# Kernel tuning notes

Measured on AMD Instinct MI355X. Metric: run time of the kernel, lower is better.

The kernel has to match this reference:

```python
import jax, jax.numpy as jnp
import numpy as np

H = 256
I = 32
O = 10


def setup_inputs() -> dict:
    key = jax.random.key(0)
    ks = jax.random.split(key, 16)
    stdv = 1.0 / np.sqrt(H)
    u = lambda k, shape: jax.random.uniform(k, shape, jnp.float32, -stdv, stdv)
    x = jax.random.normal(ks[0], (256, 512, I), jnp.float32)
    return {
        "x": x,
        "Wgx": u(ks[1], (I, H)), "Wgh": u(ks[2], (H, H)), "bg": u(ks[3], (H,)),
        "Wix": u(ks[4], (I, H)), "Wih": u(ks[5], (H, H)), "bi": u(ks[6], (H,)),
        "Wfx": u(ks[7], (I, H)), "Wfh": u(ks[8], (H, H)), "bf": u(ks[9], (H,)),
        "Wox": u(ks[10], (I, H)), "Woh": u(ks[11], (H, H)), "bo": u(ks[12], (H,)),
        "Wph": u(ks[13], (H, O)), "bp": u(ks[14], (O,)),
    }


def _lstm_forward(x, Wgx, Wgh, bg, Wix, Wih, bi, Wfx, Wfh, bf, Wox, Woh, bo, Wph, bp):
    B, S, _ = x.shape
    # Precompute all input projections in one big GEMM: (B,S,I) @ (I,4H) -> (B,S,4H)
    Wx = jnp.concatenate([Wgx, Wix, Wfx, Wox], axis=1)      # (I, 4H)
    bx = jnp.concatenate([bg, bi, bf, bo], axis=0)          # (4H,)
    xproj = jnp.einsum("bsi,ik->bsk", x, Wx) + bx           # (B, S, 4H)
    Wh = jnp.concatenate([Wgh, Wih, Wfh, Woh], axis=1)      # (H, 4H)

    # Note: torch code skips the h@Wh term at t=0; with h0=c0=0 the math is identical.
    def step(carry, xp_t):
        h, c = carry
        z = xp_t + h @ Wh                                   # (B, 4H)
        g = jnp.tanh(z[:, 0 * H:1 * H])
        i = jax.nn.sigmoid(z[:, 1 * H:2 * H])
        f = jax.nn.sigmoid(z[:, 2 * H:3 * H])
        o = jax.nn.sigmoid(z[:, 3 * H:4 * H])
        c = g * i + c * f
        h = jnp.tanh(c) * o
        return (h, c), None

    h0 = jnp.zeros((B, H), x.dtype)
    c0 = jnp.zeros((B, H), x.dtype)
    (h, _), _ = jax.lax.scan(step, (h0, c0), jnp.swapaxes(xproj, 0, 1))
    out = h @ Wph + bp                                      # (B, O)
    return jax.nn.softmax(out, axis=1)


def reference(x, Wgx, Wgh, bg, Wix, Wih, bi, Wfx, Wfh, bf, Wox, Woh, bo, Wph, bp):
    return _lstm_forward(x, Wgx, Wgh, bg, Wix, Wih, bi, Wfx, Wfh, bf, Wox, Woh, bo, Wph, bp)
```

## Files before the change

kernel.cpp:

```cpp
#include <hip/hip_runtime.h>

#define HD 256
#define ID 32
#define OD 10
#define SEQ 512
#define NBG 16
#define FLAGS_OFF 589824
#define HX_OFF    622592
#define SMEM_BYTES (16384 + 65536)

typedef __attribute__((ext_vector_type(4))) float f32x4;
typedef __attribute__((ext_vector_type(8))) unsigned short u16x8;
typedef __attribute__((ext_vector_type(8))) __bf16 bf16x8;

static __device__ __forceinline__ unsigned short f2bf(float f) {
  unsigned u = __builtin_bit_cast(unsigned, f);
  u += 0x7fffu + ((u >> 16) & 1u);
  return (unsigned short)(u >> 16);
}
static __device__ __forceinline__ float bf2f(unsigned short s) {
  unsigned u = ((unsigned)s) << 16;
  return __builtin_bit_cast(float, u);
}
static __device__ __forceinline__ f32x4 mfma16(u16x8 a, u16x8 b, f32x4 c) {
  return __builtin_amdgcn_mfma_f32_16x16x32_bf16(
      __builtin_bit_cast(bf16x8, a), __builtin_bit_cast(bf16x8, b), c, 0, 0, 0);
}
static __device__ __forceinline__ float fast_sigmoid(float x) {
  return 1.f / (1.f + __expf(-x));
}
static __device__ __forceinline__ float fast_tanh(float x) {
  return 1.f - 2.f / (__expf(2.f * x) + 1.f);
}

__global__ void pack_w(const float* __restrict__ Wgx, const float* __restrict__ Wgh,
                       const float* __restrict__ Wix, const float* __restrict__ Wih,
                       const float* __restrict__ Wfx, const float* __restrict__ Wfh,
                       const float* __restrict__ Wox, const float* __restrict__ Woh,
                       unsigned short* __restrict__ Wpk) {
  int p = blockIdx.x * blockDim.x + threadIdx.x;
  if (p >= 576 * 64) return;
  int f = p >> 6, l = p & 63;
  int hw = f / 36, r = f % 36;
  int g = r / 9, kt = r % 9;
  int U = hw * 16 + (l & 15);
  const float* Wx[4] = {Wgx, Wix, Wfx, Wox};
  const float* Wh[4] = {Wgh, Wih, Wfh, Woh};
  u16x8 v;
  #pragma unroll
  for (int i = 0; i < 8; ++i) {
    int k = kt * 32 + 8 * (l >> 4) + i;
    float val = (k < ID) ? Wx[g][k * HD + U] : Wh[g][(k - ID) * HD + U];
    v[i] = f2bf(val);
  }
  *(u16x8*)(Wpk + ((size_t)f << 9) + (l << 3)) = v;
}

template <int HF>
static __device__ __forceinline__ void mfma_own(
    const u16x8 (&wf)[4][7], const unsigned short* wlds_w, int l,
    const u16x8& ax, const u16x8 (&aown)[4], f32x4 (&acc)[4], bool full) {
  #pragma unroll
  for (int g = 0; g < 4; ++g) acc[g] = mfma16(ax, wf[g][0], acc[g]);
  if (!full) return;
  #pragma unroll
  for (int k2 = 0; k2 < 4; ++k2) {
    const int kt = 1 + 4 * HF + k2;
    #pragma unroll
    for (int g = 0; g < 4; ++g) {
      u16x8 bw;
      if (kt <= 6) bw = wf[g][kt];
      else bw = *(const u16x8*)(wlds_w + (g * 2 + (kt - 7)) * 512 + l * 8);
      acc[g] = mfma16(aown[k2], bw, acc[g]);
    }
  }
}
template <int HF>
static __device__ __forceinline__ void mfma_part(
    const u16x8 (&wf)[4][7], const unsigned short* wlds_w, int l,
    const u16x8 (&apart)[4], f32x4 (&acc)[4]) {
  #pragma unroll
  for (int k2 = 0; k2 < 4; ++k2) {
    const int kt = 1 + 4 * (1 - HF) + k2;
    #pragma unroll
    for (int g = 0; g < 4; ++g) {
      u16x8 bw;
      if (kt <= 6) bw = wf[g][kt];
      else bw = *(const u16x8*)(wlds_w + (g * 2 + (kt - 7)) * 512 + l * 8);
      acc[g] = mfma16(apart[k2], bw, acc[g]);
    }
  }
}

__global__ void __launch_bounds__(512, 2) lstm_rec(
    const float* __restrict__ x, const unsigned short* __restrict__ Wpk,
    const float* __restrict__ bgp, const float* __restrict__ bip,
    const float* __restrict__ bfp, const float* __restrict__ bop,
    const float* __restrict__ Wph, const float* __restrict__ bpp,
    unsigned int* __restrict__ flags, void* __restrict__ hx,
    float* __restrict__ out) {
  extern __shared__ __align__(16) char smem[];
  unsigned short* hbuf = (unsigned short*)smem;
  unsigned short* wlds = (unsigned short*)(smem + 16384);

  const int tid = threadIdx.x;
  const int w = tid >> 6, l = tid & 63;
  const int l15 = l & 15, l4 = l >> 4;
  const int bgi = blockIdx.x & 15, hf = blockIdx.x >> 4;
  const int b0 = bgi * 16;
  char* hxc = (char*)hx;
  unsigned int* myflag = flags + (bgi * 2 + hf) * 32;
  unsigned int* pflag  = flags + (bgi * 2 + (1 - hf)) * 32;

  const unsigned short* wbase =
      Wpk + (((size_t)(hf * 8 + w) * 36) << 9) + (l << 3);
  unsigned short* wlds_w = wlds + w * 4096;

  #pragma unroll
  for (int g = 0; g < 4; ++g)
    #pragma unroll
    for (int d = 0; d < 2; ++d) {
      u16x8 v = *(const u16x8*)(wbase + ((size_t)(g * 9 + 7 + d) << 9));
      *(u16x8*)(wlds_w + (g * 2 + d) * 512 + l * 8) = v;
    }
  u16x8 wf[4][7];
  #pragma unroll
  for (int g = 0; g < 4; ++g)
    #pragma unroll
    for (int kt = 0; kt < 7; ++kt)
      wf[g][kt] = *(const u16x8*)(wbase + ((size_t)(g * 9 + kt) << 9));

  float bias[4];
  {
    const float* bs[4] = {bgp, bip, bfp, bop};
    #pragma unroll
    for (int g = 0; g < 4; ++g) bias[g] = bs[g][hf * 128 + w * 16 + l15];
  }
  float cst[4] = {0.f, 0.f, 0.f, 0.f};

  const float* xrow = x + ((size_t)(b0 + l15) * SEQ) * ID + 8 * l4;
  float4 xv0 = *(const float4*)xrow;
  float4 xv1 = *(const float4*)(xrow + 4);

  const int ro = tid >> 5, u0 = (tid & 31) * 4;
  const int pgu = hf * 128 + u0;
  const int pofs = ro * 256 + ((((pgu >> 3) ^ ro) & 31) * 8) + (pgu & 7);

  __syncthreads();

  #pragma unroll 1
  for (int t = 0; t < SEQ; ++t) {
    u16x8 ax;
    ax[0] = f2bf(xv0.x); ax[1] = f2bf(xv0.y); ax[2] = f2bf(xv0.z); ax[3] = f2bf(xv0.w);
    ax[4] = f2bf(xv1.x); ax[5] = f2bf(xv1.y); ax[6] = f2bf(xv1.z); ax[7] = f2bf(xv1.w);
    {
      int tn = (t + 1 < SEQ) ? (t + 1) : t;
      xv0 = *(const float4*)(xrow + (size_t)tn * ID);
      xv1 = *(const float4*)(xrow + (size_t)tn * ID + 4);
    }

    const int pr = (t - 1) & 1;
    u16x8 aown[4], apart[4];
    if (t > 0) {
      while (__hip_atomic_load(pflag, __ATOMIC_RELAXED,
                               __HIP_MEMORY_SCOPE_AGENT) < (unsigned)t) {}
      __builtin_amdgcn_fence(__ATOMIC_ACQUIRE, "agent");
      const unsigned short* pp = (const unsigned short*)
          (hxc + (size_t)((pr * NBG + bgi) * 2 + (1 - hf)) * 4096) + l15 * 128;
      #pragma unroll
      for (int k2 = 0; k2 < 4; ++k2)
        apart[k2] = *(const u16x8*)(pp + 32 * k2 + 8 * l4);
      const unsigned short* hb = hbuf + pr * 4096 + l15 * 256;
      #pragma unroll
      for (int k2 = 0; k2 < 4; ++k2) {
        int c = 4 * (4 * hf + k2) + l4;
        aown[k2] = *(const u16x8*)(hb + ((c ^ l15) & 31) * 8);
      }
    }

    f32x4 acc[4];
    #pragma unroll
    for (int g = 0; g < 4; ++g)
      acc[g] = f32x4{bias[g], bias[g], bias[g], bias[g]};
    if (hf == 0) mfma_own<0>(wf, wlds_w, l, ax, aown, acc, t > 0);
    else         mfma_own<1>(wf, wlds_w, l, ax, aown, acc, t > 0);
    if (t > 0) {
      if (hf == 0) mfma_part<0>(wf, wlds_w, l, apart, acc);
      else         mfma_part<1>(wf, wlds_w, l, apart, acc);
    }

    unsigned short* ho = hbuf + (t & 1) * 4096;
    int ul = 16 * w + l15;
    #pragma unroll
    for (int i = 0; i < 4; ++i) {
      float gg = fast_tanh(acc[0][i]);
      float ii = fast_sigmoid(acc[1][i]);
      float ff = fast_sigmoid(acc[2][i]);
      float oo = fast_sigmoid(acc[3][i]);
      float cc = gg * ii + cst[i] * ff;
      cst[i] = cc;
      float hh = fast_tanh(cc) * oo;
      int r = 4 * l4 + i;
      int gu = hf * 128 + ul;
      ho[r * 256 + (((gu >> 3) ^ r) & 31) * 8 + (gu & 7)] = f2bf(hh);
    }
    __syncthreads();

    {
      unsigned long long v = *(const unsigned long long*)(ho + pofs);
      unsigned long long* dst = (unsigned long long*)
          (hxc + (size_t)(((t & 1) * NBG + bgi) * 2 + hf) * 4096);
      dst[(ro * 128 + u0) >> 2] = v;
    }
    __syncthreads();
    if (tid == 0)
      __hip_atomic_store(myflag, (unsigned)(t + 1), __ATOMIC_RELEASE,
                         __HIP_MEMORY_SCOPE_AGENT);
  }

  if (hf == 0) {
    if (w == 0) {
      while (__hip_atomic_load(pflag, __ATOMIC_RELAXED,
                               __HIP_MEMORY_SCOPE_AGENT) < (unsigned)SEQ) {}
      __builtin_amdgcn_fence(__ATOMIC_ACQUIRE, "agent");
      const unsigned short* pp = (const unsigned short*)
          (hxc + (size_t)((1 * NBG + bgi) * 2 + 1) * 4096);
      int er = l >> 2, eu0 = (l & 3) * 32;
      #pragma unroll
      for (int q = 0; q < 4; ++q) {
        u16x8 v = *(const u16x8*)(pp + er * 128 + eu0 + 8 * q);
        int gu = 128 + eu0 + 8 * q;
        *(u16x8*)(hbuf + 4096 + er * 256 + (((gu >> 3) ^ er) & 31) * 8) = v;
      }
    }
    __syncthreads();
    float* lbuf = (float*)(smem + 16384);
    if (tid < 16 * OD) {
      int eb = tid & 15, ej = tid >> 4;
      float s = bpp[ej];
      for (int k = 0; k < HD; ++k)
        s += bf2f(hbuf[4096 + eb * 256 + (((k >> 3) ^ eb) & 31) * 8 + (k & 7)]) *
             Wph[k * OD + ej];
      lbuf[eb * OD + ej] = s;
    }
    __syncthreads();
    if (tid < 16) {
      float m = -1e30f;
      #pragma unroll
      for (int j = 0; j < OD; ++j) m = fmaxf(m, lbuf[tid * OD + j]);
      float e[OD], sum = 0.f;
      #pragma unroll
      for (int j = 0; j < OD; ++j) { e[j] = __expf(lbuf[tid * OD + j] - m); sum += e[j]; }
      float inv = 1.f / sum;
      #pragma unroll
      for (int j = 0; j < OD; ++j) out[(b0 + tid) * OD + j] = e[j] * inv;
    }
  }
}

extern "C" void kernel_launch(void* const* d_in, const int* in_sizes, int n_in,
                              void* d_out, int out_size, void* d_ws, size_t ws_size,
                              hipStream_t stream) {
  const float* X   = (const float*)d_in[0];
  const float* Wgx = (const float*)d_in[1];
  const float* Wgh = (const float*)d_in[2];
  const float* bg  = (const float*)d_in[3];
  const float* Wix = (const float*)d_in[4];
  const float* Wih = (const float*)d_in[5];
  const float* bi  = (const float*)d_in[6];
  const float* Wfx = (const float*)d_in[7];
  const float* Wfh = (const float*)d_in[8];
  const float* bf  = (const float*)d_in[9];
  const float* Wox = (const float*)d_in[10];
  const float* Woh = (const float*)d_in[11];
  const float* bo  = (const float*)d_in[12];
  const float* Wph = (const float*)d_in[13];
  const float* bp  = (const float*)d_in[14];

  unsigned short* Wpk   = (unsigned short*)d_ws;
  unsigned int*   flags = (unsigned int*)((char*)d_ws + FLAGS_OFF);
  void*           hx    = (char*)d_ws + HX_OFF;

  hipMemsetAsync((char*)d_ws + FLAGS_OFF, 0, 32 * 32 * 4, stream);
  (void)hipFuncSetAttribute((const void*)lstm_rec,
                            hipFuncAttributeMaxDynamicSharedMemorySize,
                            SMEM_BYTES);

  pack_w<<<dim3(72), dim3(512), 0, stream>>>(Wgx, Wgh, Wix, Wih, Wfx, Wfh,
                                             Wox, Woh, Wpk);
  lstm_rec<<<dim3(32), dim3(512), SMEM_BYTES, stream>>>(
      X, Wpk, bg, bi, bf, bo, Wph, bp, flags, hx, (float*)d_out);
}
```

Before: 2.204 ms.

## Replace flag-based handoff with step-tagged h values polled directly

Drops the separate per-block flag and its release/acquire handshake. Each bf16 h value is now stored in global memory packed with its timestep tag in a 32-bit word, and the partner block polls those words until every tag matches. The partner loads are issued before the own-half MFMAs and only awaited afterwards, so the global read latency overlaps with compute. This also removes one __syncthreads and the staging copy through LDS. In exchange the exchanged data doubles in size, the correctness depends on relaxed-order stores being seen by uncached (sc0 sc1) loads, and the LDS h buffer now holds only this block's own half.

```diff
diff --git a/kernel.cpp b/kernel.cpp
--- a/kernel.cpp
+++ b/kernel.cpp
@@ -5,11 +5,11 @@
 #define OD 10
 #define SEQ 512
 #define NBG 16
-#define FLAGS_OFF 589824
-#define HX_OFF    622592
-#define SMEM_BYTES (16384 + 65536)
+#define HX_OFF 589824
+#define SMEM_BYTES (8192 + 65536)
 
 typedef __attribute__((ext_vector_type(4))) float f32x4;
+typedef __attribute__((ext_vector_type(4))) unsigned int u32x4;
 typedef __attribute__((ext_vector_type(8))) unsigned short u16x8;
 typedef __attribute__((ext_vector_type(8))) __bf16 bf16x8;
 
@@ -31,6 +31,32 @@
 }
 static __device__ __forceinline__ float fast_tanh(float x) {
   return 1.f - 2.f / (__expf(2.f * x) + 1.f);
+}
+
+static __device__ __forceinline__ void issue8(const void* pa,
+    u32x4& w0, u32x4& w1, u32x4& w2, u32x4& w3,
+    u32x4& w4, u32x4& w5, u32x4& w6, u32x4& w7) {
+  asm volatile(
+      "global_load_dwordx4 %0, %8, off sc0 sc1\n\t"
+      "global_load_dwordx4 %1, %8, off offset:16 sc0 sc1\n\t"
+      "global_load_dwordx4 %2, %8, off offset:128 sc0 sc1\n\t"
+      "global_load_dwordx4 %3, %8, off offset:144 sc0 sc1\n\t"
+      "global_load_dwordx4 %4, %8, off offset:256 sc0 sc1\n\t"
+      "global_load_dwordx4 %5, %8, off offset:272 sc0 sc1\n\t"
+      "global_load_dwordx4 %6, %8, off offset:384 sc0 sc1\n\t"
+      "global_load_dwordx4 %7, %8, off offset:400 sc0 sc1"
+      : "=&v"(w0), "=&v"(w1), "=&v"(w2), "=&v"(w3),
+        "=&v"(w4), "=&v"(w5), "=&v"(w6), "=&v"(w7)
+      : "v"(pa)
+      : "memory");
+}
+static __device__ __forceinline__ void awaitv(
+    u32x4& w0, u32x4& w1, u32x4& w2, u32x4& w3,
+    u32x4& w4, u32x4& w5, u32x4& w6, u32x4& w7) {
+  asm volatile("s_waitcnt vmcnt(0)"
+      : "+v"(w0), "+v"(w1), "+v"(w2), "+v"(w3),
+        "+v"(w4), "+v"(w5), "+v"(w6), "+v"(w7)
+      :: "memory");
 }
 
 __global__ void pack_w(const float* __restrict__ Wgx, const float* __restrict__ Wgh,
@@ -97,11 +123,10 @@
     const float* __restrict__ bgp, const float* __restrict__ bip,
     const float* __restrict__ bfp, const float* __restrict__ bop,
     const float* __restrict__ Wph, const float* __restrict__ bpp,
-    unsigned int* __restrict__ flags, void* __restrict__ hx,
-    float* __restrict__ out) {
+    void* __restrict__ hx, float* __restrict__ out) {
   extern __shared__ __align__(16) char smem[];
   unsigned short* hbuf = (unsigned short*)smem;
-  unsigned short* wlds = (unsigned short*)(smem + 16384);
+  unsigned short* wlds = (unsigned short*)(smem + 8192);
 
   const int tid = threadIdx.x;
   const int w = tid >> 6, l = tid & 63;
@@ -109,8 +134,6 @@
   const int bgi = blockIdx.x & 15, hf = blockIdx.x >> 4;
   const int b0 = bgi * 16;
   char* hxc = (char*)hx;
-  unsigned int* myflag = flags + (bgi * 2 + hf) * 32;
-  unsigned int* pflag  = flags + (bgi * 2 + (1 - hf)) * 32;
 
   const unsigned short* wbase =
       Wpk + (((size_t)(hf * 8 + w) * 36) << 9) + (l << 3);
@@ -141,10 +164,6 @@
   const float* xrow = x + ((size_t)(b0 + l15) * SEQ) * ID + 8 * l4;
   float4 xv0 = *(const float4*)xrow;
   float4 xv1 = *(const float4*)(xrow + 4);
-
-  const int ro = tid >> 5, u0 = (tid & 31) * 4;
-  const int pgu = hf * 128 + u0;
-  const int pofs = ro * 256 + ((((pgu >> 3) ^ ro) & 31) * 8) + (pgu & 7);
 
   __syncthreads();
 
@@ -159,22 +178,18 @@
       xv1 = *(const float4*)(xrow + (size_t)tn * ID + 4);
     }
 
-    const int pr = (t - 1) & 1;
-    u16x8 aown[4], apart[4];
+    u16x8 aown[4];
+    u32x4 w0, w1, w2, w3, w4, w5, w6, w7;
+    const char* pa = hxc +
+        ((((size_t)((t - 1) & 1)) * NBG + bgi) * 2 + (1 - hf)) * 8192 +
+        l15 * 512 + l4 * 32;
     if (t > 0) {
-      while (__hip_atomic_load(pflag, __ATOMIC_RELAXED,
-                               __HIP_MEMORY_SCOPE_AGENT) < (unsigned)t) {}
-      __builtin_amdgcn_fence(__ATOMIC_ACQUIRE, "agent");
-      const unsigned short* pp = (const unsigned short*)
-          (hxc + (size_t)((pr * NBG + bgi) * 2 + (1 - hf)) * 4096) + l15 * 128;
-      #pragma unroll
-      for (int k2 = 0; k2 < 4; ++k2)
-        apart[k2] = *(const u16x8*)(pp + 32 * k2 + 8 * l4);
-      const unsigned short* hb = hbuf + pr * 4096 + l15 * 256;
+      issue8(pa, w0, w1, w2, w3, w4, w5, w6, w7);
+      const unsigned short* hb = hbuf + ((t - 1) & 1) * 2048 + l15 * 128;
       #pragma unroll
       for (int k2 = 0; k2 < 4; ++k2) {
-        int c = 4 * (4 * hf + k2) + l4;
-        aown[k2] = *(const u16x8*)(hb + ((c ^ l15) & 31) * 8);
+        int c = 4 * k2 + l4;
+        aown[k2] = *(const u16x8*)(hb + ((c ^ l15) & 15) * 8);
       }
     }
 
@@ -184,12 +199,39 @@
       acc[g] = f32x4{bias[g], bias[g], bias[g], bias[g]};
     if (hf == 0) mfma_own<0>(wf, wlds_w, l, ax, aown, acc, t > 0);
     else         mfma_own<1>(wf, wlds_w, l, ax, aown, acc, t > 0);
+
     if (t > 0) {
+      awaitv(w0, w1, w2, w3, w4, w5, w6, w7);
+      const unsigned st = (unsigned)t;
+      #define CK(W) (((W.x ^ st) & 0xffffu) | ((W.y ^ st) & 0xffffu) | \
+                     ((W.z ^ st) & 0xffffu) | ((W.w ^ st) & 0xffffu))
+      unsigned bad = CK(w0) | CK(w1) | CK(w2) | CK(w3) |
+                     CK(w4) | CK(w5) | CK(w6) | CK(w7);
+      while (!__all(bad == 0)) {
+        __builtin_amdgcn_s_sleep(1);
+        issue8(pa, w0, w1, w2, w3, w4, w5, w6, w7);
+        awaitv(w0, w1, w2, w3, w4, w5, w6, w7);
+        bad = CK(w0) | CK(w1) | CK(w2) | CK(w3) |
+              CK(w4) | CK(w5) | CK(w6) | CK(w7);
+      }
+      #undef CK
+      u16x8 apart[4];
+      #define UNP(k2, A, B) { u32x4 d_;                       \
+        d_.x = (A.x >> 16) | (A.y & 0xffff0000u);             \
+        d_.y = (A.z >> 16) | (A.w & 0xffff0000u);             \
+        d_.z = (B.x >> 16) | (B.y & 0xffff0000u);             \
+        d_.w = (B.z >> 16) | (B.w & 0xffff0000u);             \
+        apart[k2] = __builtin_bit_cast(u16x8, d_); }
+      UNP(0, w0, w1) UNP(1, w2, w3) UNP(2, w4, w5) UNP(3, w6, w7)
+      #undef UNP
       if (hf == 0) mfma_part<0>(wf, wlds_w, l, apart, acc);
       else         mfma_part<1>(wf, wlds_w, l, apart, acc);
     }
 
-    unsigned short* ho = hbuf + (t & 1) * 4096;
+    unsigned short* ho = hbuf + (t & 1) * 2048;
+    unsigned int* hxw = (unsigned int*)(hxc +
+        ((((size_t)(t & 1)) * NBG + bgi) * 2 + hf) * 8192);
+    const unsigned stp = (unsigned)(t + 1);
     int ul = 16 * w + l15;
     #pragma unroll
     for (int i = 0; i < 4; ++i) {
@@ -200,47 +242,51 @@
       float cc = gg * ii + cst[i] * ff;
       cst[i] = cc;
       float hh = fast_tanh(cc) * oo;
+      unsigned short me = f2bf(hh);
       int r = 4 * l4 + i;
-      int gu = hf * 128 + ul;
-      ho[r * 256 + (((gu >> 3) ^ r) & 31) * 8 + (gu & 7)] = f2bf(hh);
+      ho[r * 128 + (((ul >> 3) ^ r) & 15) * 8 + (ul & 7)] = me;
+      __hip_atomic_store(hxw + r * 128 + ul, ((unsigned)me << 16) | stp,
+                         __ATOMIC_RELAXED, __HIP_MEMORY_SCOPE_AGENT);
+    }
+    __builtin_amdgcn_sched_barrier(0);
+    asm volatile("s_waitcnt lgkmcnt(0)" ::: "memory");
+    __builtin_amdgcn_s_barrier();
+    __builtin_amdgcn_sched_barrier(0);
+  }
+
+  if (hf == 0) {
+    unsigned short* hfin = (unsigned short*)(smem + 8192);
+    for (int idx = tid; idx < 2048; idx += 512) {
+      int row = idx >> 7, uo = idx & 127;
+      hfin[row * 256 + uo] =
+          hbuf[2048 + row * 128 + (((uo >> 3) ^ row) & 15) * 8 + (uo & 7)];
+    }
+    {
+      const char* pe = hxc + (((size_t)1 * NBG + bgi) * 2 + 1) * 8192 + tid * 16;
+      u32x4 e;
+      for (;;) {
+        asm volatile(
+            "global_load_dwordx4 %0, %1, off sc0 sc1\n\t"
+            "s_waitcnt vmcnt(0)"
+            : "=&v"(e) : "v"(pe) : "memory");
+        unsigned bad = ((e.x ^ 512u) & 0xffffu) | ((e.y ^ 512u) & 0xffffu) |
+                       ((e.z ^ 512u) & 0xffffu) | ((e.w ^ 512u) & 0xffffu);
+        if (__all(bad == 0)) break;
+        __builtin_amdgcn_s_sleep(1);
+      }
+      int row = tid >> 5, ul0 = (tid & 31) * 4;
+      hfin[row * 256 + 128 + ul0 + 0] = (unsigned short)(e.x >> 16);
+      hfin[row * 256 + 128 + ul0 + 1] = (unsigned short)(e.y >> 16);
+      hfin[row * 256 + 128 + ul0 + 2] = (unsigned short)(e.z >> 16);
+      hfin[row * 256 + 128 + ul0 + 3] = (unsigned short)(e.w >> 16);
     }
     __syncthreads();
-
-    {
-      unsigned long long v = *(const unsigned long long*)(ho + pofs);
-      unsigned long long* dst = (unsigned long long*)
-          (hxc + (size_t)(((t & 1) * NBG + bgi) * 2 + hf) * 4096);
-      dst[(ro * 128 + u0) >> 2] = v;
-    }
-    __syncthreads();
-    if (tid == 0)
-      __hip_atomic_store(myflag, (unsigned)(t + 1), __ATOMIC_RELEASE,
-                         __HIP_MEMORY_SCOPE_AGENT);
-  }
-
-  if (hf == 0) {
-    if (w == 0) {
-      while (__hip_atomic_load(pflag, __ATOMIC_RELAXED,
-                               __HIP_MEMORY_SCOPE_AGENT) < (unsigned)SEQ) {}
-      __builtin_amdgcn_fence(__ATOMIC_ACQUIRE, "agent");
-      const unsigned short* pp = (const unsigned short*)
-          (hxc + (size_t)((1 * NBG + bgi) * 2 + 1) * 4096);
-      int er = l >> 2, eu0 = (l & 3) * 32;
-      #pragma unroll
-      for (int q = 0; q < 4; ++q) {
-        u16x8 v = *(const u16x8*)(pp + er * 128 + eu0 + 8 * q);
-        int gu = 128 + eu0 + 8 * q;
-        *(u16x8*)(hbuf + 4096 + er * 256 + (((gu >> 3) ^ er) & 31) * 8) = v;
-      }
-    }
-    __syncthreads();
-    float* lbuf = (float*)(smem + 16384);
+    float* lbuf = (float*)(smem + 8192 + 16384);
     if (tid < 16 * OD) {
       int eb = tid & 15, ej = tid >> 4;
       float s = bpp[ej];
       for (int k = 0; k < HD; ++k)
-        s += bf2f(hbuf[4096 + eb * 256 + (((k >> 3) ^ eb) & 31) * 8 + (k & 7)]) *
-             Wph[k * OD + ej];
+        s += bf2f(hfin[eb * 256 + k]) * Wph[k * OD + ej];
       lbuf[eb * OD + ej] = s;
     }
     __syncthreads();
@@ -277,11 +323,10 @@
   const float* Wph = (const float*)d_in[13];
   const float* bp  = (const float*)d_in[14];
 
-  unsigned short* Wpk   = (unsigned short*)d_ws;
-  unsigned int*   flags = (unsigned int*)((char*)d_ws + FLAGS_OFF);
-  void*           hx    = (char*)d_ws + HX_OFF;
-
-  hipMemsetAsync((char*)d_ws + FLAGS_OFF, 0, 32 * 32 * 4, stream);
+  unsigned short* Wpk = (unsigned short*)d_ws;
+  void*           hx  = (char*)d_ws + HX_OFF;
+
+  hipMemsetAsync((char*)d_ws + HX_OFF, 0, 2 * NBG * 2 * 8192, stream);
   (void)hipFuncSetAttribute((const void*)lstm_rec,
                             hipFuncAttributeMaxDynamicSharedMemorySize,
                             SMEM_BYTES);
@@ -289,5 +334,5 @@
   pack_w<<<dim3(72), dim3(512), 0, stream>>>(Wgx, Wgh, Wix, Wih, Wfx, Wfh,
                                              Wox, Woh, Wpk);
   lstm_rec<<<dim3(32), dim3(512), SMEM_BYTES, stream>>>(
-      X, Wpk, bg, bi, bf, bo, Wph, bp, flags, hx, (float*)d_out);
-}
+      X, Wpk, bg, bi, bf, bo, Wph, bp, hx, (float*)d_out);
+}
```

New measurement: 2.915 ms. 32.3% more time.
